# Kernel optimization log

Hardware: AMD Instinct MI355X
Metric: run time of the kernel (lower is better)

Reference implementation:

```python
import jax, jax.numpy as jnp
import numpy as np

DIM = 1024
HEADS = 16
HEAD_DIM = DIM // HEADS
DFF = 4 * DIM
BASE_THETA, K_DOP, K_NOR, K_SERO = 0.5, 0.2, 0.15, 0.1
EPS = 1e-5


def _layernorm(x, g, b):
    mu = jnp.mean(x, axis=-1, keepdims=True)
    var = jnp.var(x, axis=-1, keepdims=True)
    return (x - mu) * jax.lax.rsqrt(var + EPS) * g + b


def setup_inputs() -> dict:
    key = jax.random.key(0)
    ks = jax.random.split(key, 16)
    s = 0.02
    d = {
        'x': jax.random.normal(ks[0], (2, 2048, DIM), dtype=jnp.float32),
        'ln1_g': jnp.ones((DIM,), jnp.float32),
        'ln1_b': jnp.zeros((DIM,), jnp.float32),
        'qkv_w': jax.random.normal(ks[1], (DIM, 3 * DIM), jnp.float32) * s,
        'qkv_b': jnp.zeros((3 * DIM,), jnp.float32),
        'proj_w': jax.random.normal(ks[2], (DIM, DIM), jnp.float32) * s,
        'proj_b': jnp.zeros((DIM,), jnp.float32),
        'kq_w': jax.random.normal(ks[3], (DIM, DIM), jnp.float32) * s,
        'kq_b': jnp.zeros((DIM,), jnp.float32),
        'kk_w': jax.random.normal(ks[4], (DIM, DIM), jnp.float32) * s,
        'kk_b': jnp.zeros((DIM,), jnp.float32),
        'kv_w': jax.random.normal(ks[5], (DIM, DIM), jnp.float32) * s,
        'kv_b': jnp.zeros((DIM,), jnp.float32),
        'ko_w': jax.random.normal(ks[6], (DIM, DIM), jnp.float32) * s,
        'ko_b': jnp.zeros((DIM,), jnp.float32),
        'ln2_g': jnp.ones((DIM,), jnp.float32),
        'ln2_b': jnp.zeros((DIM,), jnp.float32),
        'fc1_w': jax.random.normal(ks[7], (DIM, DFF), jnp.float32) * s,
        'fc1_b': jnp.zeros((DFF,), jnp.float32),
        'fc2_w': jax.random.normal(ks[8], (DFF, DIM), jnp.float32) * s,
        'fc2_b': jnp.zeros((DIM,), jnp.float32),
    }
    return d


def _mha(x, qkv_w, qkv_b, proj_w, proj_b):
    B, N, C = x.shape
    qkv = (x @ qkv_w + qkv_b).reshape(B, N, 3, HEADS, HEAD_DIM)
    q, k, v = qkv[:, :, 0], qkv[:, :, 1], qkv[:, :, 2]  # [B,N,H,Hd]
    scale = HEAD_DIM ** -0.5
    attn = jnp.einsum('bnhd,bmhd->bhnm', q, k) * scale
    attn = jax.nn.softmax(attn, axis=-1)
    out = jnp.einsum('bhnm,bmhd->bnhd', attn, v).reshape(B, N, C)
    return out @ proj_w + proj_b


def _kernel_attn(x, kq_w, kq_b, kk_w, kk_b, kv_w, kv_b, ko_w, ko_b):
    q = x @ kq_w + kq_b
    k = x @ kk_w + kk_b
    v = x @ kv_w + kv_b
    qk = jnp.einsum('bnc,bmc->bnm', q, k)
    theta = (BASE_THETA + K_DOP * jax.nn.sigmoid(qk)
             + K_NOR * jnp.tanh(qk) + K_SERO * jax.nn.relu(qk))
    attn = jax.nn.softmax(theta, axis=-1)
    out = jnp.einsum('bnm,bmc->bnc', attn, v)
    return out @ ko_w + ko_b


def reference(x, ln1_g, ln1_b, qkv_w, qkv_b, proj_w, proj_b,
              kq_w, kq_b, kk_w, kk_b, kv_w, kv_b, ko_w, ko_b,
              ln2_g, ln2_b, fc1_w, fc1_b, fc2_w, fc2_b):
    x = x + _mha(_layernorm(x, ln1_g, ln1_b), qkv_w, qkv_b, proj_w, proj_b)
    x = x + _kernel_attn(x, kq_w, kq_b, kk_w, kk_b, kv_w, kv_b, ko_w, ko_b)
    h = _layernorm(x, ln2_g, ln2_b)
    h = jax.nn.gelu(h @ fc1_w + fc1_b, approximate=False) @ fc2_w + fc2_b
    return x + h
```

## Files before the change

### kernel.cpp

```cpp
#include <hip/hip_runtime.h>
#include <math.h>


#define DIMC   1024
#define NTOK   4096
#define SEQ    2048
#define NHEADS 16
#define DFFC   4096
#define QSCALE 0.125f

typedef unsigned short u16;
typedef __attribute__((ext_vector_type(8))) short s16x8;
typedef __attribute__((ext_vector_type(4))) float f32x4;
#define MFMA16(a,b,c) __builtin_amdgcn_mfma_f32_16x16x32_bf16(a,b,c,0,0,0)

__device__ __forceinline__ float b2f(u16 u){ return __uint_as_float(((unsigned int)u)<<16); }
__device__ __forceinline__ u16 f2b(float f){
  unsigned int u = __float_as_uint(f);
  u += 0x7fffu + ((u>>16)&1u);
  return (u16)(u>>16);
}
__device__ __forceinline__ unsigned int pkbf(float a, float b){
  unsigned int r;
  asm("v_cvt_pk_bf16_f32 %0, %1, %2" : "=v"(r) : "v"(a), "v"(b));
  return r;
}

__device__ __forceinline__ float ldIn(const void* base, long idx, int f32){
  return f32 ? ((const float*)base)[idx] : b2f(((const u16*)base)[idx]);
}
__device__ __forceinline__ float4 ldIn4(const void* base, long idx, int f32){
  if (f32) return *(const float4*)((const float*)base + idx);
  ushort4 u = *(const ushort4*)((const u16*)base + idx);
  return make_float4(b2f(u.x), b2f(u.y), b2f(u.z), b2f(u.w));
}
__device__ __forceinline__ void ld8(const void* base, long idx, int f32, float* v){
  if (f32){
    float4 a = *(const float4*)((const float*)base + idx);
    float4 b = *(const float4*)((const float*)base + idx + 4);
    v[0]=a.x; v[1]=a.y; v[2]=a.z; v[3]=a.w;
    v[4]=b.x; v[5]=b.y; v[6]=b.z; v[7]=b.w;
  } else {
    ushort4 a = *(const ushort4*)((const u16*)base + idx);
    ushort4 b = *(const ushort4*)((const u16*)base + idx + 4);
    v[0]=b2f(a.x); v[1]=b2f(a.y); v[2]=b2f(a.z); v[3]=b2f(a.w);
    v[4]=b2f(b.x); v[5]=b2f(b.y); v[6]=b2f(b.z); v[7]=b2f(b.w);
  }
}
__device__ __forceinline__ void st8(void* base, long idx, int f32, const float* v){
  if (f32){
    *(float4*)((float*)base + idx)     = make_float4(v[0],v[1],v[2],v[3]);
    *(float4*)((float*)base + idx + 4) = make_float4(v[4],v[5],v[6],v[7]);
  } else {
    unsigned int q0 = (unsigned int)f2b(v[0]) | ((unsigned int)f2b(v[1])<<16);
    unsigned int q1 = (unsigned int)f2b(v[2]) | ((unsigned int)f2b(v[3])<<16);
    unsigned int q2 = (unsigned int)f2b(v[4]) | ((unsigned int)f2b(v[5])<<16);
    unsigned int q3 = (unsigned int)f2b(v[6]) | ((unsigned int)f2b(v[7])<<16);
    *(uint4*)((u16*)base + idx) = make_uint4(q0,q1,q2,q3);
  }
}

__device__ __forceinline__ float waveSum(float v){
  #pragma unroll
  for (int off=32; off>0; off>>=1) v += __shfl_xor(v, off, 64);
  return v;
}

__device__ __forceinline__ void async16(const u16* g, u16* l){
  __builtin_amdgcn_global_load_lds(
      (const __attribute__((address_space(1))) unsigned int*)g,
      (__attribute__((address_space(3))) unsigned int*)l, 16, 0, 0);
}

__global__ void detect_kernel(const void* ones, int* flag){
  if (threadIdx.x == 0 && blockIdx.x == 0){
    unsigned int w = *(const unsigned int*)ones;
    *flag = (w == 0x3F803F80u) ? 0 : 1;
  }
}

__global__ __launch_bounds__(256)
void transpose_w(const void* __restrict__ in, u16* __restrict__ out,
                 const int* __restrict__ flagp, int K, int N)
{
  __shared__ u16 t[32][36];
  const int fl = *flagp;
  const int n0 = blockIdx.x*32, k0 = blockIdx.y*32;
  const int tx = threadIdx.x & 31, ty = threadIdx.x >> 5;
  #pragma unroll
  for (int r = ty; r < 32; r += 8)
    t[r][tx] = f2b(ldIn(in, (long)(k0+r)*N + n0 + tx, fl));
  __syncthreads();
  #pragma unroll
  for (int r = ty; r < 32; r += 8)
    out[(long)(n0+r)*K + k0 + tx] = t[tx][r];
}

__global__ __launch_bounds__(256)
void transpose_w3(const void* in0, const void* in1, const void* in2,
                  u16* __restrict__ out, const int* __restrict__ flagp)
{
  __shared__ u16 t[32][36];
  const int fl = *flagp;
  const void* in = (blockIdx.z==0) ? in0 : ((blockIdx.z==1) ? in1 : in2);
  u16* o = out + (long)blockIdx.z*1048576L;
  const int n0 = blockIdx.x*32, k0 = blockIdx.y*32;
  const int tx = threadIdx.x & 31, ty = threadIdx.x >> 5;
  #pragma unroll
  for (int r = ty; r < 32; r += 8)
    t[r][tx] = f2b(ldIn(in, (long)(k0+r)*1024 + n0 + tx, fl));
  __syncthreads();
  #pragma unroll
  for (int r = ty; r < 32; r += 8)
    o[(long)(n0+r)*1024 + k0 + tx] = t[tx][r];
}

__global__ __launch_bounds__(256)
void transpose_b(const u16* __restrict__ in, u16* __restrict__ out,
                 int K, int N, long sIn, long sOut)
{
  __shared__ u16 t[32][36];
  const long zi = (long)blockIdx.z*sIn, zo = (long)blockIdx.z*sOut;
  const int n0 = blockIdx.x*32, k0 = blockIdx.y*32;
  const int tx = threadIdx.x & 31, ty = threadIdx.x >> 5;
  #pragma unroll
  for (int r = ty; r < 32; r += 8)
    t[r][tx] = in[zi + (long)(k0+r)*N + n0 + tx];
  __syncthreads();
  #pragma unroll
  for (int r = ty; r < 32; r += 8)
    out[zo + (long)(n0+r)*K + k0 + tx] = t[tx][r];
}

__global__ __launch_bounds__(256)
void conv_bf16(const void* __restrict__ in, u16* __restrict__ out,
               const int* __restrict__ flagp)
{
  const int fl = *flagp;
  long i = ((long)blockIdx.x*256 + threadIdx.x)*4;
  float4 v = ldIn4(in, i, fl);
  ushort4 o; o.x=f2b(v.x); o.y=f2b(v.y); o.z=f2b(v.z); o.w=f2b(v.w);
  *(ushort4*)(out+i) = o;
}

template<int BM, int MODE, int ACT>
__global__ __launch_bounds__(256)
void gemm_mfma(const u16* __restrict__ A, const u16* __restrict__ BT,
               const void* __restrict__ bias, const void* __restrict__ bias2,
               const void* __restrict__ bias3, const void* res,
               void* C, u16* Cv, const int* __restrict__ flagp, int cExt,
               int M, int N, int K, int lda, int ldb, int ldc,
               long sA, long sB, long sC)
{
  constexpr int DEPTH = (BM==128) ? 1 : 3;
  constexpr int BUFS = (BM+128)*64;
  constexpr int ST   = BM*132;
  constexpr int LSZ  = (DEPTH*BUFS > ST) ? DEPTH*BUFS : ST;
  __shared__ u16 lds[LSZ];

  const int fl = *flagp;
  const int fC = cExt ? fl : 0;
  const int z = blockIdx.z;
  A += (long)z*sA; BT += (long)z*sB;
  const long coff = (long)z*sC;
  const int m0 = blockIdx.x*BM, n0 = blockIdx.y*128;
  const int tid = threadIdx.x, w = tid>>6, l = tid&63;
  const int lr = l&15, lq = l>>4;
  constexpr int FM = BM/32;
  constexpr int NIA = BM/32;
  const int wm = (w&1)*(BM/2), wn = (w>>1)*64;

  const int rq = l>>3;
  const int cperm = (l&7) ^ rq;
  const u16* pa = A  + (long)(m0 + rq)*lda + cperm*8;
  const u16* pb = BT + (long)(n0 + rq)*ldb + cperm*8;

  f32x4 acc[FM][4];
  f32x4 osum[FM];
  #pragma unroll
  for (int i=0;i<FM;i++){
    osum[i] = (f32x4){0.f,0.f,0.f,0.f};
    #pragma unroll
    for (int j=0;j<4;j++) acc[i][j] = (f32x4){0.f,0.f,0.f,0.f};
  }

  auto stage = [&](u16* buf){
    u16* As = buf;
    u16* Bs = buf + BM*64;
    #pragma unroll
    for (int p=0;p<NIA;p++){
      const int ia = p*4 + w;
      async16(pa + (long)ia*8*lda, &As[ia*512]);
    }
    #pragma unroll
    for (int p=0;p<4;p++){
      const int ib = p*4 + w;
      async16(pb + (long)ib*8*ldb, &Bs[ib*512]);
    }
    pa += 64; pb += 64;
  };

  auto compute = [&](const u16* As){
    const u16* Bs = As + BM*64;
    const int swz = lr & 7;
    #pragma unroll
    for (int h=0; h<2; h++){
      s16x8 af[FM], bf[4];
      const int slot = ((h*4 + lq) ^ swz) << 3;
      #pragma unroll
      for (int i=0;i<FM;i++)
        af[i] = *(const s16x8*)&As[(wm + i*16 + lr)*64 + slot];
      #pragma unroll
      for (int j=0;j<4;j++)
        bf[j] = *(const s16x8*)&Bs[(wn + j*16 + lr)*64 + slot];
      __builtin_amdgcn_s_setprio(1);
      #pragma unroll
      for (int i=0;i<FM;i++)
        #pragma unroll
        for (int j=0;j<4;j++) acc[i][j] = MFMA16(af[i], bf[j], acc[i][j]);
      if constexpr (MODE==5){
        const s16x8 onesv = (s16x8){0x3F80,0x3F80,0x3F80,0x3F80,
                                    0x3F80,0x3F80,0x3F80,0x3F80};
        #pragma unroll
        for (int i=0;i<FM;i++) osum[i] = MFMA16(af[i], onesv, osum[i]);
      }
      __builtin_amdgcn_s_setprio(0);
    }
  };

  const int nk = K >> 6;

  if constexpr (DEPTH == 3){
    auto waitL = [&](){
      asm volatile("s_waitcnt vmcnt(6)" ::: "memory");
      __builtin_amdgcn_s_barrier();
    };
    stage(lds);
    stage(lds + BUFS);
    int cur = 0;
    for (int t = 0; t < nk-2; ++t){
      waitL();
      int nxt = cur+2; if (nxt >= 3) nxt -= 3;
      stage(lds + nxt*BUFS);
      compute(lds + cur*BUFS);
      cur = (cur==2) ? 0 : cur+1;
    }
    waitL();
    compute(lds + cur*BUFS);
    cur = (cur==2) ? 0 : cur+1;
    asm volatile("s_waitcnt vmcnt(0)" ::: "memory");
    __builtin_amdgcn_s_barrier();
    compute(lds + cur*BUFS);
    __syncthreads();
  } else {
    for (int t = 0; t < nk; ++t){
      stage(lds);
      asm volatile("s_waitcnt vmcnt(0)" ::: "memory");
      __builtin_amdgcn_s_barrier();
      compute(lds);
      __syncthreads();
    }
  }

  if constexpr (MODE==5){
    #pragma unroll
    for (int i=0;i<FM;i++)
      #pragma unroll
      for (int r=0;r<4;r++){
        float inv = 1.f / osum[i][r];
        #pragma unroll
        for (int j=0;j<4;j++) acc[i][j][r] *= inv;
      }
  }

  #pragma unroll
  for (int i=0;i<FM;i++)
    #pragma unroll
    for (int j=0;j<4;j++)
      #pragma unroll
      for (int r=0;r<4;r++)
        lds[(wm + i*16 + lq*4 + r)*132 + wn + j*16 + lr] = f2b(acc[i][j][r]);
  __syncthreads();

  const int trow = tid >> 4, tcol = (tid & 15)*8;
  const int gcol = n0 + tcol;
  #pragma unroll
  for (int p=0; p<BM/16; p++){
    const int row = p*16 + trow;
    const long grow = m0 + row;
    float v[8];
    #pragma unroll
    for (int e=0;e<8;e++) v[e] = b2f(lds[row*132 + tcol + e]);

    if (MODE == 2){
      #pragma unroll
      for (int e=0;e<8;e++){
        float q = v[e];
        float sig = 1.f/(1.f+__expf(-q));
        float th  = 1.f - 2.f/(__expf(2.f*q)+1.f);
        v[e] = __expf(0.5f + 0.2f*sig + 0.15f*th + 0.1f*fmaxf(q,0.f));
      }
      st8(C, coff + grow*ldc + gcol, 0, v);
    } else if (MODE == 1){
      if (n0 < 2048){
        const void* bb = (n0 < 1024) ? bias : bias2;
        const int cofs = (n0 < 1024) ? 0 : 1024;
        float bv[8]; ld8(bb, gcol - cofs, fl, bv);
        #pragma unroll
        for (int e=0;e<8;e++) v[e] += bv[e];
        st8(C, grow*2048 + gcol, 0, v);
      } else {
        float bv[8]; ld8(bias3, gcol - 2048, fl, bv);
        #pragma unroll
        for (int e=0;e<8;e++) v[e] += bv[e];
        st8(Cv, grow*1024 + (gcol - 2048), 0, v);
      }
    } else {
      if (bias){
        float bv[8]; ld8(bias, gcol, fl, bv);
        #pragma unroll
        for (int e=0;e<8;e++) v[e] += bv[e];
      }
      if (MODE == 3 && gcol < 1024){
        #pragma unroll
        for (int e=0;e<8;e++) v[e] *= QSCALE;
      }
      if (ACT==1){
        #pragma unroll
        for (int e=0;e<8;e++){
          float u = v[e];
          float y = 1.5957691216f*u*(1.f + 0.044715f*u*u);
          v[e] = u / (1.f + __expf(-y));
        }
      }
      const long idx = coff + grow*ldc + gcol;
      if (res){
        float rv[8]; ld8(res, idx, fl, rv);
        #pragma unroll
        for (int e=0;e<8;e++) v[e] += rv[e];
      }
      st8(C, idx, fC, v);
    }
  }
}

__global__ __launch_bounds__(256)
void ln_kernel(const void* __restrict__ in, const void* __restrict__ g,
               const void* __restrict__ b, u16* __restrict__ outp,
               const int* __restrict__ flagp, int inFlagged)
{
  const int fl = *flagp;
  const int fin = inFlagged ? fl : 0;
  const int row = blockIdx.x;
  const int tid = threadIdx.x;
  float4 xv = ldIn4(in, (long)row*DIMC + tid*4, fin);
  float v0=xv.x, v1=xv.y, v2=xv.z, v3=xv.w;
  float s  = v0+v1+v2+v3;
  float s2 = v0*v0+v1*v1+v2*v2+v3*v3;
  s = waveSum(s); s2 = waveSum(s2);
  __shared__ float sh[8];
  int w = tid>>6, ln = tid&63;
  if (ln==0){ sh[w]=s; sh[4+w]=s2; }
  __syncthreads();
  float ts  = sh[0]+sh[1]+sh[2]+sh[3];
  float ts2 = sh[4]+sh[5]+sh[6]+sh[7];
  float mu  = ts * (1.f/1024.f);
  float var = ts2 * (1.f/1024.f) - mu*mu;
  float rs  = rsqrtf(var + 1e-5f);
  int c = tid*4;
  float4 gv = ldIn4(g, c, fl);
  float4 bv = ldIn4(b, c, fl);
  ushort4 o;
  o.x = f2b((v0-mu)*rs*gv.x + bv.x);
  o.y = f2b((v1-mu)*rs*gv.y + bv.y);
  o.z = f2b((v2-mu)*rs*gv.z + bv.z);
  o.w = f2b((v3-mu)*rs*gv.w + bv.w);
  *(ushort4*)(outp + (long)row*DIMC + c) = o;
}

__global__ __launch_bounds__(512)
void mha_flash(const u16* __restrict__ qkv, u16* __restrict__ outp)
{
  __shared__ u16 Kl[64][72];
  __shared__ u16 Vt[64][72];
  __shared__ u16 Pl[8][16][72];
  const int h  = blockIdx.y;
  const int bb = blockIdx.z;
  const int q0 = blockIdx.x * 128;
  const int tid = threadIdx.x, lane = tid & 63, w = tid >> 6;
  const int lr = lane & 15, lq = lane >> 4;
  const long tokBase = (long)bb * SEQ;

  s16x8 qf0, qf1;
  {
    const u16* qp = qkv + (tokBase + q0 + w*16 + lr)*3072 + h*64 + lq*8;
    qf0 = *(const s16x8*)qp;
    qf1 = *(const s16x8*)(qp + 32);
  }
  f32x4 o[4];
  #pragma unroll
  for (int d=0;d<4;d++) o[d] = (f32x4){0.f,0.f,0.f,0.f};
  f32x4 osum = (f32x4){0.f,0.f,0.f,0.f};
  const s16x8 onesv = (s16x8){0x3F80,0x3F80,0x3F80,0x3F80,0x3F80,0x3F80,0x3F80,0x3F80};

  const int kk = tid >> 3, kd = (tid & 7) * 8;
  const bool doV = (tid < 256);
  const int p2 = tid & 31, dg = (tid >> 5) & 7;

  uint4 kr, vA, vB;
  const u16* kbase = qkv + (tokBase + kk)*3072 + 1024 + h*64 + kd;
  const u16* vbase = qkv + (tokBase + 2*p2)*3072 + 2048 + h*64 + dg*8;

  auto ldKV = [&](int k0){
    kr = *(const uint4*)(kbase + (long)k0*3072);
    if (doV){
      const u16* vp = vbase + (long)k0*3072;
      vA = *(const uint4*)vp;
      vB = *(const uint4*)(vp + 3072);
    }
  };
  auto wrKV = [&](){
    *(uint4*)&Kl[kk][kd] = kr;
    if (doV){
      unsigned int pk;
      #pragma unroll
      for (int jj=0;jj<4;jj++){
        pk = ((const u16*)&vA)[jj] | ((unsigned int)((const u16*)&vB)[jj] << 16);
        *(unsigned int*)&Vt[dg*8+jj][2*p2] = pk;
        pk = ((const u16*)&vA)[4+jj] | ((unsigned int)((const u16*)&vB)[4+jj] << 16);
        *(unsigned int*)&Vt[dg*8+4+jj][2*p2] = pk;
      }
    }
  };

  ldKV(0);
  for (int k0 = 0; k0 < SEQ; k0 += 64){
    __syncthreads();
    wrKV();
    if (k0 + 64 < SEQ) ldKV(k0 + 64);
    __syncthreads();

    f32x4 s[4];
    #pragma unroll
    for (int c=0;c<4;c++){
      s[c] = (f32x4){0.f,0.f,0.f,0.f};
      s16x8 kf0 = *(const s16x8*)&Kl[c*16+lr][lq*8];
      s16x8 kf1 = *(const s16x8*)&Kl[c*16+lr][lq*8+32];
      __builtin_amdgcn_s_setprio(1);
      s[c] = MFMA16(qf0, kf0, s[c]);
      s[c] = MFMA16(qf1, kf1, s[c]);
      __builtin_amdgcn_s_setprio(0);
    }
    #pragma unroll
    for (int c=0;c<4;c++){
      float p0 = __expf(s[c][0]);
      float p1 = __expf(s[c][1]);
      float p2v = __expf(s[c][2]);
      float p3 = __expf(s[c][3]);
      unsigned int a01 = pkbf(p0, p1);
      unsigned int a23 = pkbf(p2v, p3);
      u16* pr = &Pl[w][lq*4][c*16+lr];
      pr[0]   = (u16)a01;
      pr[72]  = (u16)(a01>>16);
      pr[144] = (u16)a23;
      pr[216] = (u16)(a23>>16);
    }
    s16x8 pf0 = *(const s16x8*)&Pl[w][lr][lq*8];
    s16x8 pf1 = *(const s16x8*)&Pl[w][lr][32+lq*8];
    __builtin_amdgcn_s_setprio(1);
    osum = MFMA16(pf0, onesv, osum);
    osum = MFMA16(pf1, onesv, osum);
    __builtin_amdgcn_s_setprio(0);
    #pragma unroll
    for (int d=0;d<4;d++){
      s16x8 vf0 = *(const s16x8*)&Vt[d*16+lr][lq*8];
      s16x8 vf1 = *(const s16x8*)&Vt[d*16+lr][32+lq*8];
      __builtin_amdgcn_s_setprio(1);
      o[d] = MFMA16(pf0, vf0, o[d]);
      o[d] = MFMA16(pf1, vf1, o[d]);
      __builtin_amdgcn_s_setprio(0);
    }
  }

  #pragma unroll
  for (int r=0;r<4;r++){
    float inv = 1.f / osum[r];
    long row = (tokBase + q0 + w*16 + lq*4 + r) * (long)DIMC + h*64;
    unsigned int pk01 = pkbf(o[0][r]*inv, o[1][r]*inv);
    unsigned int pk23 = pkbf(o[2][r]*inv, o[3][r]*inv);
    outp[row + lr     ] = (u16)pk01;
    outp[row + lr + 16] = (u16)(pk01>>16);
    outp[row + lr + 32] = (u16)pk23;
    outp[row + lr + 48] = (u16)(pk23>>16);
  }
}

extern "C" void kernel_launch(void* const* d_in, const int* in_sizes, int n_in,
                              void* d_out, int out_size, void* d_ws, size_t ws_size,
                              hipStream_t stream)
{
  const void* x      = d_in[0];
  const void* ln1_g  = d_in[1];
  const void* ln1_b  = d_in[2];
  const void* qkv_w  = d_in[3];
  const void* qkv_b  = d_in[4];
  const void* proj_w = d_in[5];
  const void* proj_b = d_in[6];
  const void* kq_w   = d_in[7];
  const void* kq_b   = d_in[8];
  const void* kk_w   = d_in[9];
  const void* kk_b   = d_in[10];
  const void* kv_w   = d_in[11];
  const void* kv_b   = d_in[12];
  const void* ko_w   = d_in[13];
  const void* ko_b   = d_in[14];
  const void* ln2_g  = d_in[15];
  const void* ln2_b  = d_in[16];
  const void* fc1_w  = d_in[17];
  const void* fc1_b  = d_in[18];
  const void* fc2_w  = d_in[19];
  const void* fc2_b  = d_in[20];

  int* flag = (int*)d_ws;
  u16* Ar   = (u16*)((char*)d_ws + 64);
  u16* B0   = Ar + 4194304L;
  u16* QK   = B0;
  u16* Vt   = B0 + 8388608L;
  u16* C0   = B0 + 12582912L;
  u16* Sb   = C0;
  u16* WT   = C0;
  u16* vtmp = C0 + 4194304L;
  u16* WT2  = C0 + 4194304L;
  u16* FC1  = B0;
  u16* Qr   = B0;

  dim3 blk(256);
  const void* np = nullptr;

  detect_kernel<<<1, 64, 0, stream>>>(ln1_g, flag);
  transpose_w<<<dim3(96,32), blk, 0, stream>>>(qkv_w, WT, flag, DIMC, 3*DIMC);
  ln_kernel<<<NTOK, blk, 0, stream>>>(x, ln1_g, ln1_b, Ar, flag, 1);
  gemm_mfma<128,3,0><<<dim3(32,24,1), blk, 0, stream>>>(
      Ar, WT, qkv_b, np, np, np, Qr, nullptr, flag, 0,
      NTOK, 3*DIMC, DIMC, DIMC, DIMC, 3*DIMC, 0,0,0);
  mha_flash<<<dim3(SEQ/128, NHEADS, 2), dim3(512), 0, stream>>>(Qr, Ar);
  transpose_w<<<dim3(32,32), blk, 0, stream>>>(proj_w, WT, flag, DIMC, DIMC);
  gemm_mfma<64,0,0><<<dim3(64,8,1), blk, 0, stream>>>(
      Ar, WT, proj_b, np, np, x, d_out, nullptr, flag, 1,
      NTOK, DIMC, DIMC, DIMC, DIMC, DIMC, 0,0,0);
  conv_bf16<<<NTOK, blk, 0, stream>>>(d_out, Ar, flag);
  transpose_w3<<<dim3(32,32,3), blk, 0, stream>>>(kq_w, kk_w, kv_w, WT, flag);
  gemm_mfma<128,1,0><<<dim3(32,24,1), blk, 0, stream>>>(
      Ar, WT, kq_b, kk_b, kv_b, np, QK, vtmp, flag, 0,
      NTOK, 3*DIMC, DIMC, DIMC, DIMC, 2048, 0,0,0);
  transpose_b<<<dim3(32,64,2), blk, 0, stream>>>(
      vtmp, Vt, SEQ, DIMC, 2097152L, 2097152L);
  gemm_mfma<128,2,0><<<dim3(16,16,2), blk, 0, stream>>>(
      QK, QK + 1024, np, np, np, np, Sb, nullptr, flag, 0,
      SEQ, SEQ, DIMC, 2048, 2048, SEQ, 4194304L, 4194304L, 4194304L);
  gemm_mfma<64,5,0><<<dim3(32,8,2), blk, 0, stream>>>(
      Sb, Vt, np, np, np, np, Ar, nullptr, flag, 0,
      SEQ, DIMC, SEQ, SEQ, SEQ, DIMC, 4194304L, 2097152L, 2097152L);
  transpose_w<<<dim3(32,32), blk, 0, stream>>>(ko_w, WT, flag, DIMC, DIMC);
  gemm_mfma<64,0,0><<<dim3(64,8,1), blk, 0, stream>>>(
      Ar, WT, ko_b, np, np, d_out, d_out, nullptr, flag, 1,
      NTOK, DIMC, DIMC, DIMC, DIMC, DIMC, 0,0,0);
  ln_kernel<<<NTOK, blk, 0, stream>>>(d_out, ln2_g, ln2_b, Ar, flag, 1);
  transpose_w<<<dim3(128,32), blk, 0, stream>>>(fc1_w, WT2, flag, DIMC, DFFC);
  gemm_mfma<128,0,1><<<dim3(32,32,1), blk, 0, stream>>>(
      Ar, WT2, fc1_b, np, np, np, FC1, nullptr, flag, 0,
      NTOK, DFFC, DIMC, DIMC, DIMC, DFFC, 0,0,0);
  transpose_w<<<dim3(32,128), blk, 0, stream>>>(fc2_w, WT2, flag, DFFC, DIMC);
  gemm_mfma<64,0,0><<<dim3(64,8,1), blk, 0, stream>>>(
      FC1, WT2, fc2_b, np, np, d_out, d_out, nullptr, flag, 1,
      NTOK, DIMC, DFFC, DFFC, DFFC, DIMC, 0,0,0);
}
```

Before: 597.5 us.

## Fuse V transpose and bf16 conversion into GEMM epilogues, double-buffer flash K/V

The KV projection GEMM now writes the V block transposed straight into the Vt layout through LDS, which removes the separate transpose_b kernel. A new MODE 4 for the proj GEMM also stores a bf16 copy of the residual output, which removes the conv_bf16 kernel. The MHA flash kernel double-buffers its K/V LDS tiles to drop one barrier per iteration. The kernel-attention score epilogue computes sigmoid and tanh from one shared exp using hardware reciprocals. These changes cut launches and memory round-trips, but the transposed LDS writes may cause bank conflicts and the fast reciprocal loses a little precision.

```diff
diff --git a/kernel.cpp b/kernel.cpp
--- a/kernel.cpp
+++ b/kernel.cpp
@@ -23,6 +23,11 @@
 __device__ __forceinline__ unsigned int pkbf(float a, float b){
   unsigned int r;
   asm("v_cvt_pk_bf16_f32 %0, %1, %2" : "=v"(r) : "v"(a), "v"(b));
+  return r;
+}
+__device__ __forceinline__ float frcp(float x){
+  float r;
+  asm("v_rcp_f32 %0, %1" : "=v"(r) : "v"(x));
   return r;
 }
 
@@ -113,34 +118,6 @@
   #pragma unroll
   for (int r = ty; r < 32; r += 8)
     o[(long)(n0+r)*1024 + k0 + tx] = t[tx][r];
-}
-
-__global__ __launch_bounds__(256)
-void transpose_b(const u16* __restrict__ in, u16* __restrict__ out,
-                 int K, int N, long sIn, long sOut)
-{
-  __shared__ u16 t[32][36];
-  const long zi = (long)blockIdx.z*sIn, zo = (long)blockIdx.z*sOut;
-  const int n0 = blockIdx.x*32, k0 = blockIdx.y*32;
-  const int tx = threadIdx.x & 31, ty = threadIdx.x >> 5;
-  #pragma unroll
-  for (int r = ty; r < 32; r += 8)
-    t[r][tx] = in[zi + (long)(k0+r)*N + n0 + tx];
-  __syncthreads();
-  #pragma unroll
-  for (int r = ty; r < 32; r += 8)
-    out[zo + (long)(n0+r)*K + k0 + tx] = t[tx][r];
-}
-
-__global__ __launch_bounds__(256)
-void conv_bf16(const void* __restrict__ in, u16* __restrict__ out,
-               const int* __restrict__ flagp)
-{
-  const int fl = *flagp;
-  long i = ((long)blockIdx.x*256 + threadIdx.x)*4;
-  float4 v = ldIn4(in, i, fl);
-  ushort4 o; o.x=f2b(v.x); o.y=f2b(v.y); o.z=f2b(v.z); o.w=f2b(v.w);
-  *(ushort4*)(out+i) = o;
 }
 
 template<int BM, int MODE, int ACT>
@@ -273,17 +250,39 @@
       }
   }
 
+  const bool vtr = (MODE==1) && (n0 >= 2048);
   #pragma unroll
   for (int i=0;i<FM;i++)
     #pragma unroll
     for (int j=0;j<4;j++)
       #pragma unroll
-      for (int r=0;r<4;r++)
-        lds[(wm + i*16 + lq*4 + r)*132 + wn + j*16 + lr] = f2b(acc[i][j][r]);
+      for (int r=0;r<4;r++){
+        const u16 bv16 = f2b(acc[i][j][r]);
+        if (vtr)
+          lds[(wn + j*16 + lr)*132 + wm + i*16 + lq*4 + r] = bv16;
+        else
+          lds[(wm + i*16 + lq*4 + r)*132 + wn + j*16 + lr] = bv16;
+      }
   __syncthreads();
 
   const int trow = tid >> 4, tcol = (tid & 15)*8;
   const int gcol = n0 + tcol;
+
+  if (vtr){
+    const int bidx = m0 >> 11;
+    const int tb = (m0 & 2047) + tcol;
+    #pragma unroll
+    for (int p=0; p<BM/16; p++){
+      const int ch = p*16 + trow;
+      float bv = ldIn(bias3, n0 - 2048 + ch, fl);
+      float v[8];
+      #pragma unroll
+      for (int e=0;e<8;e++) v[e] = b2f(lds[ch*132 + tcol + e]) + bv;
+      st8(Cv, (long)bidx*2097152L + (long)(n0 - 2048 + ch)*2048 + tb, 0, v);
+    }
+    return;
+  }
+
   #pragma unroll
   for (int p=0; p<BM/16; p++){
     const int row = p*16 + trow;
@@ -296,25 +295,20 @@
       #pragma unroll
       for (int e=0;e<8;e++){
         float q = v[e];
-        float sig = 1.f/(1.f+__expf(-q));
-        float th  = 1.f - 2.f/(__expf(2.f*q)+1.f);
+        float En = __expf(-q);
+        float sig = frcp(1.f + En);
+        float t2 = fminf(En*En, 3.0e38f);
+        float th = (1.f - t2) * frcp(1.f + t2);
         v[e] = __expf(0.5f + 0.2f*sig + 0.15f*th + 0.1f*fmaxf(q,0.f));
       }
       st8(C, coff + grow*ldc + gcol, 0, v);
     } else if (MODE == 1){
-      if (n0 < 2048){
-        const void* bb = (n0 < 1024) ? bias : bias2;
-        const int cofs = (n0 < 1024) ? 0 : 1024;
-        float bv[8]; ld8(bb, gcol - cofs, fl, bv);
-        #pragma unroll
-        for (int e=0;e<8;e++) v[e] += bv[e];
-        st8(C, grow*2048 + gcol, 0, v);
-      } else {
-        float bv[8]; ld8(bias3, gcol - 2048, fl, bv);
-        #pragma unroll
-        for (int e=0;e<8;e++) v[e] += bv[e];
-        st8(Cv, grow*1024 + (gcol - 2048), 0, v);
-      }
+      const void* bb = (n0 < 1024) ? bias : bias2;
+      const int cofs = (n0 < 1024) ? 0 : 1024;
+      float bv[8]; ld8(bb, gcol - cofs, fl, bv);
+      #pragma unroll
+      for (int e=0;e<8;e++) v[e] += bv[e];
+      st8(C, grow*2048 + gcol, 0, v);
     } else {
       if (bias){
         float bv[8]; ld8(bias, gcol, fl, bv);
@@ -340,6 +334,8 @@
         for (int e=0;e<8;e++) v[e] += rv[e];
       }
       st8(C, idx, fC, v);
+      if (MODE == 4)
+        st8(Cv, grow*1024 + gcol, 0, v);
     }
   }
 }
@@ -381,8 +377,8 @@
 __global__ __launch_bounds__(512)
 void mha_flash(const u16* __restrict__ qkv, u16* __restrict__ outp)
 {
-  __shared__ u16 Kl[64][72];
-  __shared__ u16 Vt[64][72];
+  __shared__ u16 Kl[2][64][72];
+  __shared__ u16 Vt[2][64][72];
   __shared__ u16 Pl[8][16][72];
   const int h  = blockIdx.y;
   const int bb = blockIdx.z;
@@ -419,24 +415,24 @@
       vB = *(const uint4*)(vp + 3072);
     }
   };
-  auto wrKV = [&](){
-    *(uint4*)&Kl[kk][kd] = kr;
+  auto wrKV = [&](int bi){
+    *(uint4*)&Kl[bi][kk][kd] = kr;
     if (doV){
       unsigned int pk;
       #pragma unroll
       for (int jj=0;jj<4;jj++){
         pk = ((const u16*)&vA)[jj] | ((unsigned int)((const u16*)&vB)[jj] << 16);
-        *(unsigned int*)&Vt[dg*8+jj][2*p2] = pk;
+        *(unsigned int*)&Vt[bi][dg*8+jj][2*p2] = pk;
         pk = ((const u16*)&vA)[4+jj] | ((unsigned int)((const u16*)&vB)[4+jj] << 16);
-        *(unsigned int*)&Vt[dg*8+4+jj][2*p2] = pk;
+        *(unsigned int*)&Vt[bi][dg*8+4+jj][2*p2] = pk;
       }
     }
   };
 
   ldKV(0);
+  int bi = 0;
   for (int k0 = 0; k0 < SEQ; k0 += 64){
-    __syncthreads();
-    wrKV();
+    wrKV(bi);
     if (k0 + 64 < SEQ) ldKV(k0 + 64);
     __syncthreads();
 
@@ -444,8 +440,8 @@
     #pragma unroll
     for (int c=0;c<4;c++){
       s[c] = (f32x4){0.f,0.f,0.f,0.f};
-      s16x8 kf0 = *(const s16x8*)&Kl[c*16+lr][lq*8];
-      s16x8 kf1 = *(const s16x8*)&Kl[c*16+lr][lq*8+32];
+      s16x8 kf0 = *(const s16x8*)&Kl[bi][c*16+lr][lq*8];
+      s16x8 kf1 = *(const s16x8*)&Kl[bi][c*16+lr][lq*8+32];
       __builtin_amdgcn_s_setprio(1);
       s[c] = MFMA16(qf0, kf0, s[c]);
       s[c] = MFMA16(qf1, kf1, s[c]);
@@ -473,13 +469,14 @@
     __builtin_amdgcn_s_setprio(0);
     #pragma unroll
     for (int d=0;d<4;d++){
-      s16x8 vf0 = *(const s16x8*)&Vt[d*16+lr][lq*8];
-      s16x8 vf1 = *(const s16x8*)&Vt[d*16+lr][32+lq*8];
+      s16x8 vf0 = *(const s16x8*)&Vt[bi][d*16+lr][lq*8];
+      s16x8 vf1 = *(const s16x8*)&Vt[bi][d*16+lr][32+lq*8];
       __builtin_amdgcn_s_setprio(1);
       o[d] = MFMA16(pf0, vf0, o[d]);
       o[d] = MFMA16(pf1, vf1, o[d]);
       __builtin_amdgcn_s_setprio(0);
     }
+    bi ^= 1;
   }
 
   #pragma unroll
@@ -529,7 +526,6 @@
   u16* C0   = B0 + 12582912L;
   u16* Sb   = C0;
   u16* WT   = C0;
-  u16* vtmp = C0 + 4194304L;
   u16* WT2  = C0 + 4194304L;
   u16* FC1  = B0;
   u16* Qr   = B0;
@@ -545,16 +541,13 @@
       NTOK, 3*DIMC, DIMC, DIMC, DIMC, 3*DIMC, 0,0,0);
   mha_flash<<<dim3(SEQ/128, NHEADS, 2), dim3(512), 0, stream>>>(Qr, Ar);
   transpose_w<<<dim3(32,32), blk, 0, stream>>>(proj_w, WT, flag, DIMC, DIMC);
-  gemm_mfma<64,0,0><<<dim3(64,8,1), blk, 0, stream>>>(
-      Ar, WT, proj_b, np, np, x, d_out, nullptr, flag, 1,
+  gemm_mfma<64,4,0><<<dim3(64,8,1), blk, 0, stream>>>(
+      Ar, WT, proj_b, np, np, x, d_out, Ar, flag, 1,
       NTOK, DIMC, DIMC, DIMC, DIMC, DIMC, 0,0,0);
-  conv_bf16<<<NTOK, blk, 0, stream>>>(d_out, Ar, flag);
   transpose_w3<<<dim3(32,32,3), blk, 0, stream>>>(kq_w, kk_w, kv_w, WT, flag);
   gemm_mfma<128,1,0><<<dim3(32,24,1), blk, 0, stream>>>(
-      Ar, WT, kq_b, kk_b, kv_b, np, QK, vtmp, flag, 0,
+      Ar, WT, kq_b, kk_b, kv_b, np, QK, Vt, flag, 0,
       NTOK, 3*DIMC, DIMC, DIMC, DIMC, 2048, 0,0,0);
-  transpose_b<<<dim3(32,64,2), blk, 0, stream>>>(
-      vtmp, Vt, SEQ, DIMC, 2097152L, 2097152L);
   gemm_mfma<128,2,0><<<dim3(16,16,2), blk, 0, stream>>>(
       QK, QK + 1024, np, np, np, np, Sb, nullptr, flag, 0,
       SEQ, SEQ, DIMC, 2048, 2048, SEQ, 4194304L, 4194304L, 4194304L);
```

Result: faster. 570.5 us (-4.5%).
